# Kernel tuning notes

Hardware: AMD Instinct MI355X
Metric: run time of the kernel (lower is better)

The kernel has to match this reference:

```python
import jax, jax.numpy as jnp
import numpy as np
from jax import lax

H, MEM, AUX = 1024, 256, 16
S = MEM + AUX          # total_slots
B, T = 8, 4096
TOPK = 8               # top_k_binding
GAMMA, BETA, PTS = 0.92, 0.08, 0.4  # gamma, beta, prediction_torque_scale
RANK = 10              # coupling_rank == prediction_rank


def _inv_softplus(v):
    return float(np.log(np.expm1(max(float(v), 1e-6))))


def setup_inputs() -> dict:
    key = jax.random.key(0)
    ks = jax.random.split(key, 8)
    x = jax.random.normal(ks[0], (B, T, H), dtype=jnp.float32)
    # base basis: orthonormal columns in the first MEM slots (memory_dim < hidden_dim -> QR branch)
    q, _ = jnp.linalg.qr(jax.random.normal(ks[1], (H, MEM), dtype=jnp.float32))
    basis = jnp.zeros((H, S), jnp.float32).at[:, :MEM].set(q)
    return dict(
        x=x,
        basis=basis,
        tape_init_re=jax.random.normal(ks[2], (S,), dtype=jnp.float32) / S ** 0.5,
        tape_init_im=jax.random.normal(ks[3], (S,), dtype=jnp.float32) / S ** 0.5,
        eta_raw=jnp.asarray(_inv_softplus(0.08), jnp.float32),
        alpha=jnp.asarray(0.35, jnp.float32),
        torque_rotation=jnp.zeros((S,), jnp.float32),
        w_r=jnp.zeros((S,), jnp.float32),
        breadth_gate=jnp.zeros((S,), jnp.float32),
        epsilon_factor=jax.random.normal(ks[4], (S, RANK), dtype=jnp.float32) * 0.02,
        epsilon_scale=jnp.zeros((RANK,), jnp.float32),
        epsilon_diag=jnp.zeros((S,), jnp.float32),
        pred_factor=jax.random.normal(ks[5], (S, RANK), dtype=jnp.float32) * 0.02,
        pred_scale=jnp.zeros((RANK,), jnp.float32),
        pred_diag=jnp.zeros((S,), jnp.float32),
    )


def _forward(x, basis, tape_init_re, tape_init_im, eta_raw, alpha,
             torque_rotation, w_r, breadth_gate,
             epsilon_factor, epsilon_scale, epsilon_diag,
             pred_factor, pred_scale, pred_diag):
    active = jnp.arange(S) < MEM                      # base slots active (fixed population)
    amf = active.astype(jnp.float32)
    eta = jax.nn.softplus(eta_raw)
    # low-rank Hermitian coupling epsilon and prediction operator W_pred
    eps = (epsilon_factor * epsilon_scale) @ epsilon_factor.T + jnp.diag(epsilon_diag)
    wp = (pred_factor * pred_scale) @ pred_factor.T + jnp.diag(pred_diag)
    eps_c = eps.astype(jnp.complex64)
    wp_c = wp.astype(jnp.complex64)
    rot = jnp.exp(1j * torque_rotation.astype(jnp.complex64))  # torque phase rotation
    wr_gate = jax.nn.sigmoid(w_r)
    bg = jax.nn.sigmoid(breadth_gate)

    def renorm(tape):
        masked = tape * amf
        nrm = jnp.sqrt(jnp.maximum((jnp.abs(masked) ** 2).sum(-1, keepdims=True), 1e-16))
        return masked / nrm

    tape0 = (tape_init_re + 1j * tape_init_im) * amf   # aux slots zeroed as in _complex_tape_init
    tape0 = renorm(jnp.broadcast_to(tape0, (B, S)))

    def step(carry, x_t):
        tape, prev = carry                              # [B,S] complex64 each
        m = jnp.einsum('hs,bh->bs', basis, x_t)         # project into slot space
        mag = jnp.abs(m) * amf
        kth = lax.top_k(mag, TOPK)[0][:, -1:]           # top-k binding threshold
        inj = jnp.where((mag >= kth) & active, m, 0.0).astype(jnp.complex64)
        rotated = tape * rot
        drive = jnp.einsum('st,bt->bs', eps_c, rotated)  # coupling drive
        pred = jnp.einsum('st,bt->bs', wp_c, rotated)    # prediction torque
        new = (GAMMA * rotated + eta * drive + BETA * inj
               + PTS * 1j * pred + wr_gate * prev)
        new = renorm(new)
        y = x_t + alpha * jnp.einsum('hs,bs->bh', basis, bg * new.real)
        return (new, tape), y

    (_, _), ys = lax.scan(step, (tape0, tape0), jnp.swapaxes(x, 0, 1))
    return jnp.swapaxes(ys, 0, 1)


def reference(x, basis, tape_init_re, tape_init_im, eta_raw, alpha,
              torque_rotation, w_r, breadth_gate,
              epsilon_factor, epsilon_scale, epsilon_diag,
              pred_factor, pred_scale, pred_diag):
    return _forward(x, basis, tape_init_re, tape_init_im, eta_raw, alpha,
                    torque_rotation, w_r, breadth_gate,
                    epsilon_factor, epsilon_scale, epsilon_diag,
                    pred_factor, pred_scale, pred_diag)
```

## Files before the change

### kernel.cpp

```cpp
#include <hip/hip_runtime.h>
#include <cstdint>
#include <cstddef>

#define HD    1024
#define SLOTS 272
#define MEMS  256
#define BATCH 8
#define TT    4096
#define RR    (BATCH*TT)
#define RANKC 10

#define GAMMA 0.92f
#define BETA  0.08f
#define PTS   0.4f

typedef float f32x2 __attribute__((ext_vector_type(2)));
#define PKFMA(a, b, c) __builtin_elementwise_fma((a), (b), (c))

#define DPP_ADD(v, ctrl, rmask)                                                   \
    v += __int_as_float(__builtin_amdgcn_update_dpp(                              \
        0, __float_as_int(v), (ctrl), (rmask), 0xf, true))

__device__ __forceinline__ float wave_sum_bcast(float v)
{
    DPP_ADD(v, 0xB1,  0xf);
    DPP_ADD(v, 0x4E,  0xf);
    DPP_ADD(v, 0x141, 0xf);
    DPP_ADD(v, 0x140, 0xf);
    DPP_ADD(v, 0x142, 0xa);
    DPP_ADD(v, 0x143, 0xc);
    return __int_as_float(__builtin_amdgcn_readlane(__float_as_int(v), 63));
}

__global__ void prep_kernel(const float* __restrict__ t0re, const float* __restrict__ t0im,
                            const float* __restrict__ eta_raw,
                            const float* __restrict__ trot, const float* __restrict__ w_r,
                            const float* __restrict__ bgate,
                            const float* __restrict__ eps_scale, const float* __restrict__ pred_scale,
                            const float* __restrict__ eps_diag, const float* __restrict__ pred_diag,
                            float* __restrict__ consts, int* __restrict__ flags)
{
    __shared__ float red[MEMS];
    const int s = threadIdx.x;
    const float tr = t0re[s], ti = t0im[s];
    red[s] = tr * tr + ti * ti;
    __syncthreads();
    for (int off = 128; off > 0; off >>= 1) {
        if (s < off) red[s] += red[s + off];
        __syncthreads();
    }
    const float nrm = sqrtf(fmaxf(red[0], 1e-16f));
    const float eta = log1pf(expf(eta_raw[0]));
    const float rc = cosf(trot[s]), rs = sinf(trot[s]);
    const float c1 = GAMMA + eta * eps_diag[s];
    const float c2 = PTS * pred_diag[s];
    consts[0 * MEMS + s] = 1.0f / (1.0f + expf(-w_r[s]));
    consts[1 * MEMS + s] = 1.0f / (1.0f + expf(-bgate[s]));
    consts[2 * MEMS + s] = c1 * rc - c2 * rs;
    consts[3 * MEMS + s] = c1 * rs + c2 * rc;
    consts[4 * MEMS + s] = tr / nrm;
    consts[5 * MEMS + s] = ti / nrm;
    consts[6 * MEMS + s] = rc;
    consts[7 * MEMS + s] = rs;
    if (s == 0) {
        consts[8 * MEMS] = eta;
        int f1 = 0, f2 = 0;
        for (int k = 0; k < RANKC; ++k) {
            if (eps_scale[k]  != 0.0f) f1 = 1;
            if (pred_scale[k] != 0.0f) f2 = 1;
        }
        flags[0] = f1;
        flags[1] = f2;
    }
}

__global__ __launch_bounds__(256) void proj_kernel(const float* __restrict__ x,
                                                   const float* __restrict__ basis,
                                                   float* __restrict__ M)
{
    __shared__ float As[32][68];
    __shared__ float Bs[32][68];
    const int tid  = threadIdx.x;
    const int row0 = blockIdx.x * 64;
    const int col0 = blockIdx.y * 64;
    const int mt = tid >> 4, nt = tid & 15;
    float acc[4][4] = {};
    for (int k0 = 0; k0 < HD; k0 += 32) {
        {
            int q = tid, m = q >> 3, kq = q & 7;
            float4 a = *(const float4*)&x[(size_t)(row0 + m) * HD + k0 + kq * 4];
            As[kq * 4 + 0][m] = a.x; As[kq * 4 + 1][m] = a.y;
            As[kq * 4 + 2][m] = a.z; As[kq * 4 + 3][m] = a.w;
            q = tid + 256; m = q >> 3; kq = q & 7;
            float4 b = *(const float4*)&x[(size_t)(row0 + m) * HD + k0 + kq * 4];
            As[kq * 4 + 0][m] = b.x; As[kq * 4 + 1][m] = b.y;
            As[kq * 4 + 2][m] = b.z; As[kq * 4 + 3][m] = b.w;
            q = tid; int k = q >> 4; int nq = q & 15;
            float4 c = *(const float4*)&basis[(size_t)(k0 + k) * SLOTS + col0 + nq * 4];
            *(float4*)&Bs[k][nq * 4] = c;
            q = tid + 256; k = q >> 4; nq = q & 15;
            float4 d = *(const float4*)&basis[(size_t)(k0 + k) * SLOTS + col0 + nq * 4];
            *(float4*)&Bs[k][nq * 4] = d;
        }
        __syncthreads();
#pragma unroll
        for (int kk = 0; kk < 32; ++kk) {
            float4 a = *(const float4*)&As[kk][mt * 4];
            float4 b = *(const float4*)&Bs[kk][nt * 4];
            float av[4] = {a.x, a.y, a.z, a.w};
            float bv[4] = {b.x, b.y, b.z, b.w};
#pragma unroll
            for (int i = 0; i < 4; ++i)
#pragma unroll
                for (int j = 0; j < 4; ++j) acc[i][j] += av[i] * bv[j];
        }
        __syncthreads();
    }
#pragma unroll
    for (int i = 0; i < 4; ++i) {
        float4 o = {acc[i][0], acc[i][1], acc[i][2], acc[i][3]};
        *(float4*)&M[(size_t)(row0 + mt * 4 + i) * MEMS + col0 + nt * 4] = o;
    }
}

__global__ __launch_bounds__(64) void topk_kernel(float* __restrict__ M)
{
    const int r    = blockIdx.x;
    const int lane = threadIdx.x;
    float4 v = *(const float4*)&M[(size_t)r * MEMS + lane * 4];
    float vals[4] = {fabsf(v.x), fabsf(v.y), fabsf(v.z), fabsf(v.w)};
    float keep[4] = {vals[0], vals[1], vals[2], vals[3]};
    float kv = 0.0f;
#pragma unroll
    for (int it = 0; it < 8; ++it) {
        float lm = vals[0]; int li = 0;
#pragma unroll
        for (int j = 1; j < 4; ++j)
            if (vals[j] > lm) { lm = vals[j]; li = j; }
        float bm = lm; int bi = lane * 4 + li;
#pragma unroll
        for (int off = 1; off < 64; off <<= 1) {
            float om = __shfl_xor(bm, off);
            int   oi = __shfl_xor(bi, off);
            if (om > bm || (om == bm && oi < bi)) { bm = om; bi = oi; }
        }
        kv = bm;
        if ((bi >> 2) == lane) vals[bi & 3] = -1.0f;
    }
    float4 o;
    o.x = (keep[0] >= kv) ? BETA * v.x : 0.0f;
    o.y = (keep[1] >= kv) ? BETA * v.y : 0.0f;
    o.z = (keep[2] >= kv) ? BETA * v.z : 0.0f;
    o.w = (keep[3] >= kv) ? BETA * v.w : 0.0f;
    *(float4*)&M[(size_t)r * MEMS + lane * 4] = o;
}

__global__ __launch_bounds__(64) void scan_kernel(const float* __restrict__ M,
                                                  const float* __restrict__ consts,
                                                  const int* __restrict__ flags,
                                                  const float* __restrict__ eps_fac,
                                                  const float* __restrict__ eps_scale,
                                                  const float* __restrict__ eps_diag,
                                                  const float* __restrict__ pred_fac,
                                                  const float* __restrict__ pred_scale,
                                                  const float* __restrict__ pred_diag,
                                                  float* __restrict__ Wout)
{
    const int b    = blockIdx.x;
    const int lane = threadIdx.x;
    const int s0   = lane * 4;
    const int general = flags[0] | flags[1];
    const size_t base = (size_t)b * TT * MEMS + s0;

    if (!general) {
        f32x2 wrg[2], A2[2], B2[2], nB2[2];
        f32x2 wre[2], wim[2], qre[2], qim[2];
        {
            const float4 w4 = *(const float4*)&consts[0 * MEMS + s0];
            const float4 a4 = *(const float4*)&consts[2 * MEMS + s0];
            const float4 b4 = *(const float4*)&consts[3 * MEMS + s0];
            const float4 r4 = *(const float4*)&consts[4 * MEMS + s0];
            const float4 i4 = *(const float4*)&consts[5 * MEMS + s0];
            wrg[0] = {w4.x, w4.y};  wrg[1] = {w4.z, w4.w};
            A2[0]  = {a4.x, a4.y};  A2[1]  = {a4.z, a4.w};
            B2[0]  = {b4.x, b4.y};  B2[1]  = {b4.z, b4.w};
            nB2[0] = {-b4.x, -b4.y}; nB2[1] = {-b4.z, -b4.w};
            wre[0] = {r4.x, r4.y};  wre[1] = {r4.z, r4.w};
            wim[0] = {i4.x, i4.y};  wim[1] = {i4.z, i4.w};
            qre[0] = wre[0]; qre[1] = wre[1];
            qim[0] = wim[0]; qim[1] = wim[1];
        }
        float ssp;
        {
            const f32x2 p0 = PKFMA(wim[0], wim[0], wre[0] * wre[0]);
            const f32x2 p1 = PKFMA(wim[1], wim[1], wre[1] * wre[1]);
            const f32x2 pp = p0 + p1;
            ssp = pp.x + pp.y;
        }
        float4 mbuf[16];
#pragma unroll
        for (int j = 0; j < 16; ++j)
            mbuf[j] = *(const float4*)&M[base + (size_t)j * MEMS];
        for (int t0 = 0; t0 < TT; t0 += 16) {
#pragma unroll
            for (int j = 0; j < 16; ++j) {
                const int t = t0 + j;
                const float4 mc = mbuf[j];
                mbuf[j] = *(const float4*)&M[base + (size_t)(t + 16) * MEMS];
                const float stot = wave_sum_bcast(ssp);
                const float icv  = __builtin_amdgcn_rsqf(fmaxf(stot, 1e-16f));
                const f32x2 ic2  = {icv, icv};
                const f32x2 Lr0 = PKFMA(A2[0], wre[0], nB2[0] * wim[0]);
                const f32x2 Li0 = PKFMA(B2[0], wre[0], A2[0]  * wim[0]);
                const f32x2 Lr1 = PKFMA(A2[1], wre[1], nB2[1] * wim[1]);
                const f32x2 Li1 = PKFMA(B2[1], wre[1], A2[1]  * wim[1]);
                const f32x2 m0 = {mc.x, mc.y};
                const f32x2 m1 = {mc.z, mc.w};
                const f32x2 wqr0 = PKFMA(wrg[0], qre[0], m0);
                const f32x2 wqi0 = wrg[0] * qim[0];
                const f32x2 wqr1 = PKFMA(wrg[1], qre[1], m1);
                const f32x2 wqi1 = wrg[1] * qim[1];
                const f32x2 u1r0 = PKFMA(ic2, Lr0, wqr0);
                const f32x2 u1i0 = PKFMA(ic2, Li0, wqi0);
                const f32x2 u1r1 = PKFMA(ic2, Lr1, wqr1);
                const f32x2 u1i1 = PKFMA(ic2, Li1, wqi1);
                const f32x2 ps0 = PKFMA(u1i0, u1i0, u1r0 * u1r0);
                const f32x2 ps1 = PKFMA(u1i1, u1i1, u1r1 * u1r1);
                const f32x2 pp  = ps0 + ps1;
                const f32x2 nr0 = wre[0] * ic2, ni0 = wim[0] * ic2;
                const f32x2 nr1 = wre[1] * ic2, ni1 = wim[1] * ic2;
                const int tr = (t - 1) < 0 ? 0 : (t - 1);
                const float4 wq4 = {nr0.x, nr0.y, nr1.x, nr1.y};
                *(float4*)&Wout[base + (size_t)tr * MEMS] = wq4;
                qre[0] = nr0;  qim[0] = ni0;  qre[1] = nr1;  qim[1] = ni1;
                wre[0] = u1r0; wim[0] = u1i0; wre[1] = u1r1; wim[1] = u1i1;
                ssp = pp.x + pp.y;
            }
        }
        {
            const float stot = wave_sum_bcast(ssp);
            const float icv  = __builtin_amdgcn_rsqf(fmaxf(stot, 1e-16f));
            const float4 wq4 = {wre[0].x * icv, wre[0].y * icv,
                                wre[1].x * icv, wre[1].y * icv};
            *(float4*)&Wout[base + (size_t)(TT - 1) * MEMS] = wq4;
        }
        return;
    }

    float wr4[4], ur[4], ui[4], pr[4], pi[4];
    float rc4[4], rs4[4], ed4[4], pd4[4];
#pragma unroll
    for (int i = 0; i < 4; ++i) {
        wr4[i] = consts[0 * MEMS + s0 + i];
        ur[i]  = consts[4 * MEMS + s0 + i];
        ui[i]  = consts[5 * MEMS + s0 + i];
        pr[i] = ur[i]; pi[i] = ui[i];
        rc4[i] = consts[6 * MEMS + s0 + i];
        rs4[i] = consts[7 * MEMS + s0 + i];
        ed4[i] = eps_diag[s0 + i];
        pd4[i] = pred_diag[s0 + i];
    }
    const float eta  = consts[8 * MEMS];
    const int es_any = flags[0];
    const int ps_any = flags[1];
    float4 mbuf[4];
#pragma unroll
    for (int j = 0; j < 4; ++j)
        mbuf[j] = *(const float4*)&M[base + (size_t)j * MEMS];
    for (int t0 = 0; t0 < TT; t0 += 4) {
#pragma unroll
        for (int j = 0; j < 4; ++j) {
            const int t = t0 + j;
            const float4 mc = mbuf[j];
            mbuf[j] = *(const float4*)&M[base + (size_t)(t + 4) * MEMS];
            float rr[4], ri[4], nr[4], ni[4];
#pragma unroll
            for (int i = 0; i < 4; ++i) {
                rr[i] = ur[i] * rc4[i] - ui[i] * rs4[i];
                ri[i] = ur[i] * rs4[i] + ui[i] * rc4[i];
            }
            const float mv[4] = {mc.x, mc.y, mc.z, mc.w};
#pragma unroll
            for (int i = 0; i < 4; ++i) {
                nr[i] = GAMMA * rr[i] + wr4[i] * pr[i] + eta * ed4[i] * rr[i]
                        - PTS * pd4[i] * ri[i] + mv[i];
                ni[i] = GAMMA * ri[i] + wr4[i] * pi[i] + eta * ed4[i] * ri[i]
                        + PTS * pd4[i] * rr[i];
            }
            if (es_any) {
#pragma unroll
                for (int k = 0; k < RANKC; ++k) {
                    float u[4], prj = 0.0f, pij = 0.0f;
#pragma unroll
                    for (int i = 0; i < 4; ++i) {
                        u[i] = eps_fac[(size_t)(s0 + i) * RANKC + k];
                        prj = fmaf(u[i], rr[i], prj);
                        pij = fmaf(u[i], ri[i], pij);
                    }
                    prj = wave_sum_bcast(prj);
                    pij = wave_sum_bcast(pij);
                    const float sc = eta * eps_scale[k];
#pragma unroll
                    for (int i = 0; i < 4; ++i) {
                        nr[i] = fmaf(sc * u[i], prj, nr[i]);
                        ni[i] = fmaf(sc * u[i], pij, ni[i]);
                    }
                }
            }
            if (ps_any) {
#pragma unroll
                for (int k = 0; k < RANKC; ++k) {
                    float u[4], qrj = 0.0f, qij = 0.0f;
#pragma unroll
                    for (int i = 0; i < 4; ++i) {
                        u[i] = pred_fac[(size_t)(s0 + i) * RANKC + k];
                        qrj = fmaf(u[i], rr[i], qrj);
                        qij = fmaf(u[i], ri[i], qij);
                    }
                    qrj = wave_sum_bcast(qrj);
                    qij = wave_sum_bcast(qij);
                    const float sc = PTS * pred_scale[k];
#pragma unroll
                    for (int i = 0; i < 4; ++i) {
                        nr[i] = fmaf(-sc * u[i], qij, nr[i]);
                        ni[i] = fmaf( sc * u[i], qrj, ni[i]);
                    }
                }
            }
            float ss = 0.0f;
#pragma unroll
            for (int i = 0; i < 4; ++i) ss = fmaf(nr[i], nr[i], fmaf(ni[i], ni[i], ss));
            ss = wave_sum_bcast(ss);
            const float inv = __builtin_amdgcn_rsqf(fmaxf(ss, 1e-16f));
#pragma unroll
            for (int i = 0; i < 4; ++i) {
                pr[i] = ur[i]; pi[i] = ui[i];
                ur[i] = nr[i] * inv; ui[i] = ni[i] * inv;
            }
            const float4 wq = {ur[0], ur[1], ur[2], ur[3]};
            *(float4*)&Wout[base + (size_t)t * MEMS] = wq;
        }
    }
}

__global__ __launch_bounds__(256) void outp_kernel(const float* __restrict__ W,
                                                   const float* __restrict__ basis,
                                                   const float* __restrict__ x,
                                                   const float* __restrict__ alpha_p,
                                                   const float* __restrict__ consts,
                                                   float* __restrict__ y)
{
    __shared__ float As[32][68];
    __shared__ float Bs[32][68];
    const int tid  = threadIdx.x;
    const int row0 = blockIdx.x * 64;
    const int col0 = blockIdx.y * 64;
    const int mt = tid >> 4, nt = tid & 15;
    const float alpha = alpha_p[0];
    const float* bgc  = consts + MEMS;
    const int m0 = tid >> 3, m1 = (tid + 256) >> 3;
    const int kq0 = tid & 7;
    float acc[4][4] = {};
    for (int k0 = 0; k0 < MEMS; k0 += 32) {
        {
            const float4 bgv = *(const float4*)&bgc[k0 + kq0 * 4];
            const float bx = alpha * bgv.x, by = alpha * bgv.y;
            const float bz = alpha * bgv.z, bw = alpha * bgv.w;
            float4 a = *(const float4*)&W[(size_t)(row0 + m0) * MEMS + k0 + kq0 * 4];
            As[kq0 * 4 + 0][m0] = a.x; As[kq0 * 4 + 1][m0] = a.y;
            As[kq0 * 4 + 2][m0] = a.z; As[kq0 * 4 + 3][m0] = a.w;
            float4 b = *(const float4*)&W[(size_t)(row0 + m1) * MEMS + k0 + kq0 * 4];
            As[kq0 * 4 + 0][m1] = b.x; As[kq0 * 4 + 1][m1] = b.y;
            As[kq0 * 4 + 2][m1] = b.z; As[kq0 * 4 + 3][m1] = b.w;
            int q = tid; int n = q >> 3;
            float4 c = *(const float4*)&basis[(size_t)(col0 + n) * SLOTS + k0 + kq0 * 4];
            Bs[kq0 * 4 + 0][n] = c.x * bx; Bs[kq0 * 4 + 1][n] = c.y * by;
            Bs[kq0 * 4 + 2][n] = c.z * bz; Bs[kq0 * 4 + 3][n] = c.w * bw;
            q = tid + 256; n = q >> 3;
            float4 d = *(const float4*)&basis[(size_t)(col0 + n) * SLOTS + k0 + kq0 * 4];
            Bs[kq0 * 4 + 0][n] = d.x * bx; Bs[kq0 * 4 + 1][n] = d.y * by;
            Bs[kq0 * 4 + 2][n] = d.z * bz; Bs[kq0 * 4 + 3][n] = d.w * bw;
        }
        __syncthreads();
#pragma unroll
        for (int kk = 0; kk < 32; ++kk) {
            float4 a = *(const float4*)&As[kk][mt * 4];
            float4 b = *(const float4*)&Bs[kk][nt * 4];
            float av[4] = {a.x, a.y, a.z, a.w};
            float bv[4] = {b.x, b.y, b.z, b.w};
#pragma unroll
            for (int i = 0; i < 4; ++i)
#pragma unroll
                for (int j = 0; j < 4; ++j) acc[i][j] += av[i] * bv[j];
        }
        __syncthreads();
    }
#pragma unroll
    for (int i = 0; i < 4; ++i) {
        const size_t ro = (size_t)(row0 + mt * 4 + i) * HD + col0 + nt * 4;
        float4 xv = *(const float4*)&x[ro];
        float4 o  = {xv.x + acc[i][0], xv.y + acc[i][1],
                     xv.z + acc[i][2], xv.w + acc[i][3]};
        *(float4*)&y[ro] = o;
    }
}

extern "C" void kernel_launch(void* const* d_in, const int* in_sizes, int n_in,
                              void* d_out, int out_size, void* d_ws, size_t ws_size,
                              hipStream_t stream)
{
    const float* x          = (const float*)d_in[0];
    const float* basis      = (const float*)d_in[1];
    const float* t0re       = (const float*)d_in[2];
    const float* t0im       = (const float*)d_in[3];
    const float* eta_raw    = (const float*)d_in[4];
    const float* alpha      = (const float*)d_in[5];
    const float* trot       = (const float*)d_in[6];
    const float* w_r        = (const float*)d_in[7];
    const float* bgate      = (const float*)d_in[8];
    const float* eps_fac    = (const float*)d_in[9];
    const float* eps_scale  = (const float*)d_in[10];
    const float* eps_diag   = (const float*)d_in[11];
    const float* pred_fac   = (const float*)d_in[12];
    const float* pred_scale = (const float*)d_in[13];
    const float* pred_diag  = (const float*)d_in[14];
    float* out = (float*)d_out;

    const size_t szM = (size_t)RR * MEMS * sizeof(float);
    const size_t szW = szM;
    const size_t szC = 16384;

    char* ws = (char*)d_ws;
    float *Mbuf, *Wbuf, *cbuf;
    if (ws_size >= szM + szW + szC) {
        Mbuf = (float*)(ws);
        Wbuf = (float*)(ws + szM);
        cbuf = (float*)(ws + szM + szW);
    } else {
        Mbuf = (float*)d_out;
        Wbuf = (float*)(ws);
        cbuf = (float*)(ws + szW);
    }
    int* fbuf = (int*)(cbuf + 8 * MEMS + 16);

    prep_kernel<<<1, 256, 0, stream>>>(t0re, t0im, eta_raw, trot, w_r, bgate,
                                       eps_scale, pred_scale, eps_diag, pred_diag,
                                       cbuf, fbuf);
    proj_kernel<<<dim3(RR / 64, MEMS / 64), 256, 0, stream>>>(x, basis, Mbuf);
    topk_kernel<<<RR, 64, 0, stream>>>(Mbuf);
    scan_kernel<<<BATCH, 64, 0, stream>>>(Mbuf, cbuf, fbuf,
                                          eps_fac, eps_scale, eps_diag,
                                          pred_fac, pred_scale, pred_diag,
                                          Wbuf);
    outp_kernel<<<dim3(RR / 64, HD / 64), 256, 0, stream>>>(Wbuf, basis, x, alpha,
                                                            cbuf, out);
}
```

Before: 1.069 ms.

## Widen GEMM tiles to 64x256 and restructure scan normalization reduction

Both GEMM kernels (projection and output) switch from 64x64 tiles with K-step 32 to 64x256 tiles with K-step 16, and each thread now computes a 2x2 set of 4x4 sub-blocks. The aim is more data reuse per shared-memory load and fewer redundant reads of x and W. In the fast-path scan, the per-step norm computation is re-expressed algebraically: three partial dot products (L·L, L·W, W·W) are reduced together in one batched DPP pass, so the reduction is no longer on the serial dependency chain between steps. The cost is more registers in the GEMMs, which can lower occupancy, and slightly different floating-point rounding in the scan.

```diff
diff --git a/kernel.cpp b/kernel.cpp
--- a/kernel.cpp
+++ b/kernel.cpp
@@ -30,6 +30,18 @@
     DPP_ADD(v, 0x142, 0xa);
     DPP_ADD(v, 0x143, 0xc);
     return __int_as_float(__builtin_amdgcn_readlane(__float_as_int(v), 63));
+}
+
+__device__ __forceinline__ void wave_sum3(float& a, float& b, float& c)
+{
+#define L3(ctrl, rmask)                                                           \
+    DPP_ADD(a, ctrl, rmask); DPP_ADD(b, ctrl, rmask); DPP_ADD(c, ctrl, rmask);
+    L3(0xB1, 0xf) L3(0x4E, 0xf) L3(0x141, 0xf)
+    L3(0x140, 0xf) L3(0x142, 0xa) L3(0x143, 0xc)
+#undef L3
+    a = __int_as_float(__builtin_amdgcn_readlane(__float_as_int(a), 63));
+    b = __int_as_float(__builtin_amdgcn_readlane(__float_as_int(b), 63));
+    c = __int_as_float(__builtin_amdgcn_readlane(__float_as_int(c), 63));
 }
 
 __global__ void prep_kernel(const float* __restrict__ t0re, const float* __restrict__ t0im,
@@ -78,49 +90,61 @@
                                                    const float* __restrict__ basis,
                                                    float* __restrict__ M)
 {
-    __shared__ float As[32][68];
-    __shared__ float Bs[32][68];
+    __shared__ float As[16][64];
+    __shared__ float Bs[16][260];
     const int tid  = threadIdx.x;
     const int row0 = blockIdx.x * 64;
-    const int col0 = blockIdx.y * 64;
-    const int mt = tid >> 4, nt = tid & 15;
-    float acc[4][4] = {};
-    for (int k0 = 0; k0 < HD; k0 += 32) {
+    const int mt = tid >> 5;
+    const int nt = tid & 31;
+    const int ar = tid >> 2;
+    const int ak = (tid & 3) * 4;
+    const int bk = tid >> 4;
+    const int bn = (tid & 15) * 16;
+    float acc[2][2][4][4] = {};
+    for (int k0 = 0; k0 < HD; k0 += 16) {
         {
-            int q = tid, m = q >> 3, kq = q & 7;
-            float4 a = *(const float4*)&x[(size_t)(row0 + m) * HD + k0 + kq * 4];
-            As[kq * 4 + 0][m] = a.x; As[kq * 4 + 1][m] = a.y;
-            As[kq * 4 + 2][m] = a.z; As[kq * 4 + 3][m] = a.w;
-            q = tid + 256; m = q >> 3; kq = q & 7;
-            float4 b = *(const float4*)&x[(size_t)(row0 + m) * HD + k0 + kq * 4];
-            As[kq * 4 + 0][m] = b.x; As[kq * 4 + 1][m] = b.y;
-            As[kq * 4 + 2][m] = b.z; As[kq * 4 + 3][m] = b.w;
-            q = tid; int k = q >> 4; int nq = q & 15;
-            float4 c = *(const float4*)&basis[(size_t)(k0 + k) * SLOTS + col0 + nq * 4];
-            *(float4*)&Bs[k][nq * 4] = c;
-            q = tid + 256; k = q >> 4; nq = q & 15;
-            float4 d = *(const float4*)&basis[(size_t)(k0 + k) * SLOTS + col0 + nq * 4];
-            *(float4*)&Bs[k][nq * 4] = d;
+            const float4 av = *(const float4*)&x[(size_t)(row0 + ar) * HD + k0 + ak];
+            As[ak + 0][ar] = av.x; As[ak + 1][ar] = av.y;
+            As[ak + 2][ar] = av.z; As[ak + 3][ar] = av.w;
+#pragma unroll
+            for (int c = 0; c < 4; ++c) {
+                const float4 bv = *(const float4*)&basis[(size_t)(k0 + bk) * SLOTS + bn + c * 4];
+                *(float4*)&Bs[bk][bn + c * 4] = bv;
+            }
         }
         __syncthreads();
 #pragma unroll
-        for (int kk = 0; kk < 32; ++kk) {
-            float4 a = *(const float4*)&As[kk][mt * 4];
-            float4 b = *(const float4*)&Bs[kk][nt * 4];
-            float av[4] = {a.x, a.y, a.z, a.w};
-            float bv[4] = {b.x, b.y, b.z, b.w};
-#pragma unroll
-            for (int i = 0; i < 4; ++i)
-#pragma unroll
-                for (int j = 0; j < 4; ++j) acc[i][j] += av[i] * bv[j];
+        for (int kk = 0; kk < 16; ++kk) {
+            const float4 a0 = *(const float4*)&As[kk][mt * 4];
+            const float4 a1 = *(const float4*)&As[kk][32 + mt * 4];
+            const float4 b0 = *(const float4*)&Bs[kk][nt * 4];
+            const float4 b1 = *(const float4*)&Bs[kk][128 + nt * 4];
+            const float av[2][4] = {{a0.x, a0.y, a0.z, a0.w}, {a1.x, a1.y, a1.z, a1.w}};
+            const float bv[2][4] = {{b0.x, b0.y, b0.z, b0.w}, {b1.x, b1.y, b1.z, b1.w}};
+#pragma unroll
+            for (int p = 0; p < 2; ++p)
+#pragma unroll
+                for (int q = 0; q < 2; ++q)
+#pragma unroll
+                    for (int i = 0; i < 4; ++i)
+#pragma unroll
+                        for (int j = 0; j < 4; ++j)
+                            acc[p][q][i][j] += av[p][i] * bv[q][j];
         }
         __syncthreads();
     }
 #pragma unroll
-    for (int i = 0; i < 4; ++i) {
-        float4 o = {acc[i][0], acc[i][1], acc[i][2], acc[i][3]};
-        *(float4*)&M[(size_t)(row0 + mt * 4 + i) * MEMS + col0 + nt * 4] = o;
-    }
+    for (int p = 0; p < 2; ++p)
+#pragma unroll
+        for (int i = 0; i < 4; ++i) {
+            const int r = row0 + p * 32 + mt * 4 + i;
+#pragma unroll
+            for (int q = 0; q < 2; ++q) {
+                const float4 o = {acc[p][q][i][0], acc[p][q][i][1],
+                                  acc[p][q][i][2], acc[p][q][i][3]};
+                *(float4*)&M[(size_t)r * MEMS + q * 128 + nt * 4] = o;
+            }
+        }
 }
 
 __global__ __launch_bounds__(64) void topk_kernel(float* __restrict__ M)
@@ -173,7 +197,7 @@
     const size_t base = (size_t)b * TT * MEMS + s0;
 
     if (!general) {
-        f32x2 wrg[2], A2[2], B2[2], nB2[2];
+        f32x2 wrg[2], A2[2], B2[2];
         f32x2 wre[2], wim[2], qre[2], qim[2];
         {
             const float4 w4 = *(const float4*)&consts[0 * MEMS + s0];
@@ -184,19 +208,12 @@
             wrg[0] = {w4.x, w4.y};  wrg[1] = {w4.z, w4.w};
             A2[0]  = {a4.x, a4.y};  A2[1]  = {a4.z, a4.w};
             B2[0]  = {b4.x, b4.y};  B2[1]  = {b4.z, b4.w};
-            nB2[0] = {-b4.x, -b4.y}; nB2[1] = {-b4.z, -b4.w};
             wre[0] = {r4.x, r4.y};  wre[1] = {r4.z, r4.w};
             wim[0] = {i4.x, i4.y};  wim[1] = {i4.z, i4.w};
             qre[0] = wre[0]; qre[1] = wre[1];
             qim[0] = wim[0]; qim[1] = wim[1];
         }
-        float ssp;
-        {
-            const f32x2 p0 = PKFMA(wim[0], wim[0], wre[0] * wre[0]);
-            const f32x2 p1 = PKFMA(wim[1], wim[1], wre[1] * wre[1]);
-            const f32x2 pp = p0 + p1;
-            ssp = pp.x + pp.y;
-        }
+        float icv = 1.0f;
         float4 mbuf[16];
 #pragma unroll
         for (int j = 0; j < 16; ++j)
@@ -207,39 +224,41 @@
                 const int t = t0 + j;
                 const float4 mc = mbuf[j];
                 mbuf[j] = *(const float4*)&M[base + (size_t)(t + 16) * MEMS];
-                const float stot = wave_sum_bcast(ssp);
-                const float icv  = __builtin_amdgcn_rsqf(fmaxf(stot, 1e-16f));
-                const f32x2 ic2  = {icv, icv};
-                const f32x2 Lr0 = PKFMA(A2[0], wre[0], nB2[0] * wim[0]);
-                const f32x2 Li0 = PKFMA(B2[0], wre[0], A2[0]  * wim[0]);
-                const f32x2 Lr1 = PKFMA(A2[1], wre[1], nB2[1] * wim[1]);
-                const f32x2 Li1 = PKFMA(B2[1], wre[1], A2[1]  * wim[1]);
+                const f32x2 Lr0 = PKFMA(A2[0], wre[0], -(B2[0] * wim[0]));
+                const f32x2 Li0 = PKFMA(B2[0], wre[0],  A2[0] * wim[0]);
+                const f32x2 Lr1 = PKFMA(A2[1], wre[1], -(B2[1] * wim[1]));
+                const f32x2 Li1 = PKFMA(B2[1], wre[1],  A2[1] * wim[1]);
                 const f32x2 m0 = {mc.x, mc.y};
                 const f32x2 m1 = {mc.z, mc.w};
-                const f32x2 wqr0 = PKFMA(wrg[0], qre[0], m0);
-                const f32x2 wqi0 = wrg[0] * qim[0];
-                const f32x2 wqr1 = PKFMA(wrg[1], qre[1], m1);
-                const f32x2 wqi1 = wrg[1] * qim[1];
-                const f32x2 u1r0 = PKFMA(ic2, Lr0, wqr0);
-                const f32x2 u1i0 = PKFMA(ic2, Li0, wqi0);
-                const f32x2 u1r1 = PKFMA(ic2, Lr1, wqr1);
-                const f32x2 u1i1 = PKFMA(ic2, Li1, wqi1);
-                const f32x2 ps0 = PKFMA(u1i0, u1i0, u1r0 * u1r0);
-                const f32x2 ps1 = PKFMA(u1i1, u1i1, u1r1 * u1r1);
-                const f32x2 pp  = ps0 + ps1;
-                const f32x2 nr0 = wre[0] * ic2, ni0 = wim[0] * ic2;
-                const f32x2 nr1 = wre[1] * ic2, ni1 = wim[1] * ic2;
-                const int tr = (t - 1) < 0 ? 0 : (t - 1);
-                const float4 wq4 = {nr0.x, nr0.y, nr1.x, nr1.y};
-                *(float4*)&Wout[base + (size_t)tr * MEMS] = wq4;
-                qre[0] = nr0;  qim[0] = ni0;  qre[1] = nr1;  qim[1] = ni1;
-                wre[0] = u1r0; wim[0] = u1i0; wre[1] = u1r1; wim[1] = u1i1;
-                ssp = pp.x + pp.y;
+                const f32x2 Wr0 = PKFMA(wrg[0], qre[0], m0);
+                const f32x2 Wi0 = wrg[0] * qim[0];
+                const f32x2 Wr1 = PKFMA(wrg[1], qre[1], m1);
+                const f32x2 Wi1 = wrg[1] * qim[1];
+                f32x2 el = PKFMA(Li0, Li0, Lr0 * Lr0);
+                el = PKFMA(Lr1, Lr1, el); el = PKFMA(Li1, Li1, el);
+                float pl = el.x + el.y;
+                f32x2 ex = PKFMA(Li0, Wi0, Lr0 * Wr0);
+                ex = PKFMA(Lr1, Wr1, ex); ex = PKFMA(Li1, Wi1, ex);
+                float px2 = (ex.x + ex.y) * 2.0f;
+                f32x2 ew = PKFMA(Wi0, Wi0, Wr0 * Wr0);
+                ew = PKFMA(Wr1, Wr1, ew); ew = PKFMA(Wi1, Wi1, ew);
+                float pw = ew.x + ew.y;
+                wave_sum3(pl, px2, pw);
+                const f32x2 ic2 = {icv, icv};
+                const f32x2 sr0 = wre[0] * ic2, si0 = wim[0] * ic2;
+                const f32x2 sr1 = wre[1] * ic2, si1 = wim[1] * ic2;
+                const int trow = t ? (t - 1) : 0;
+                const float4 st4 = {sr0.x, sr0.y, sr1.x, sr1.y};
+                *(float4*)&Wout[base + (size_t)trow * MEMS] = st4;
+                const f32x2 w0r = PKFMA(ic2, Lr0, Wr0), w0i = PKFMA(ic2, Li0, Wi0);
+                const f32x2 w1r = PKFMA(ic2, Lr1, Wr1), w1i = PKFMA(ic2, Li1, Wi1);
+                const float nn = fmaf(fmaf(icv, pl, px2), icv, pw);
+                icv = __builtin_amdgcn_rsqf(fmaxf(nn, 1e-16f));
+                qre[0] = sr0; qim[0] = si0; qre[1] = sr1; qim[1] = si1;
+                wre[0] = w0r; wim[0] = w0i; wre[1] = w1r; wim[1] = w1i;
             }
         }
         {
-            const float stot = wave_sum_bcast(ssp);
-            const float icv  = __builtin_amdgcn_rsqf(fmaxf(stot, 1e-16f));
             const float4 wq4 = {wre[0].x * icv, wre[0].y * icv,
                                 wre[1].x * icv, wre[1].y * icv};
             *(float4*)&Wout[base + (size_t)(TT - 1) * MEMS] = wq4;
@@ -350,59 +369,68 @@
                                                    const float* __restrict__ consts,
                                                    float* __restrict__ y)
 {
-    __shared__ float As[32][68];
-    __shared__ float Bs[32][68];
+    __shared__ float As[16][64];
+    __shared__ float Bs[16][260];
     const int tid  = threadIdx.x;
     const int row0 = blockIdx.x * 64;
-    const int col0 = blockIdx.y * 64;
-    const int mt = tid >> 4, nt = tid & 15;
+    const int col0 = blockIdx.y * 256;
+    const int mt = tid >> 5;
+    const int nt = tid & 31;
+    const int ar = tid >> 2;
+    const int ak = (tid & 3) * 4;
     const float alpha = alpha_p[0];
     const float* bgc  = consts + MEMS;
-    const int m0 = tid >> 3, m1 = (tid + 256) >> 3;
-    const int kq0 = tid & 7;
-    float acc[4][4] = {};
-    for (int k0 = 0; k0 < MEMS; k0 += 32) {
+    float acc[2][2][4][4] = {};
+    for (int k0 = 0; k0 < MEMS; k0 += 16) {
         {
-            const float4 bgv = *(const float4*)&bgc[k0 + kq0 * 4];
-            const float bx = alpha * bgv.x, by = alpha * bgv.y;
-            const float bz = alpha * bgv.z, bw = alpha * bgv.w;
-            float4 a = *(const float4*)&W[(size_t)(row0 + m0) * MEMS + k0 + kq0 * 4];
-            As[kq0 * 4 + 0][m0] = a.x; As[kq0 * 4 + 1][m0] = a.y;
-            As[kq0 * 4 + 2][m0] = a.z; As[kq0 * 4 + 3][m0] = a.w;
-            float4 b = *(const float4*)&W[(size_t)(row0 + m1) * MEMS + k0 + kq0 * 4];
-            As[kq0 * 4 + 0][m1] = b.x; As[kq0 * 4 + 1][m1] = b.y;
-            As[kq0 * 4 + 2][m1] = b.z; As[kq0 * 4 + 3][m1] = b.w;
-            int q = tid; int n = q >> 3;
-            float4 c = *(const float4*)&basis[(size_t)(col0 + n) * SLOTS + k0 + kq0 * 4];
-            Bs[kq0 * 4 + 0][n] = c.x * bx; Bs[kq0 * 4 + 1][n] = c.y * by;
-            Bs[kq0 * 4 + 2][n] = c.z * bz; Bs[kq0 * 4 + 3][n] = c.w * bw;
-            q = tid + 256; n = q >> 3;
-            float4 d = *(const float4*)&basis[(size_t)(col0 + n) * SLOTS + k0 + kq0 * 4];
-            Bs[kq0 * 4 + 0][n] = d.x * bx; Bs[kq0 * 4 + 1][n] = d.y * by;
-            Bs[kq0 * 4 + 2][n] = d.z * bz; Bs[kq0 * 4 + 3][n] = d.w * bw;
+            const float4 av = *(const float4*)&W[(size_t)(row0 + ar) * MEMS + k0 + ak];
+            As[ak + 0][ar] = av.x; As[ak + 1][ar] = av.y;
+            As[ak + 2][ar] = av.z; As[ak + 3][ar] = av.w;
+#pragma unroll
+            for (int c = 0; c < 4; ++c) {
+                const float4 bv  = *(const float4*)&basis[(size_t)(col0 + tid) * SLOTS + k0 + c * 4];
+                const float4 bg4 = *(const float4*)&bgc[k0 + c * 4];
+                Bs[c * 4 + 0][tid] = bv.x * (alpha * bg4.x);
+                Bs[c * 4 + 1][tid] = bv.y * (alpha * bg4.y);
+                Bs[c * 4 + 2][tid] = bv.z * (alpha * bg4.z);
+                Bs[c * 4 + 3][tid] = bv.w * (alpha * bg4.w);
+            }
         }
         __syncthreads();
 #pragma unroll
-        for (int kk = 0; kk < 32; ++kk) {
-            float4 a = *(const float4*)&As[kk][mt * 4];
-            float4 b = *(const float4*)&Bs[kk][nt * 4];
-            float av[4] = {a.x, a.y, a.z, a.w};
-            float bv[4] = {b.x, b.y, b.z, b.w};
-#pragma unroll
-            for (int i = 0; i < 4; ++i)
-#pragma unroll
-                for (int j = 0; j < 4; ++j) acc[i][j] += av[i] * bv[j];
+        for (int kk = 0; kk < 16; ++kk) {
+            const float4 a0 = *(const float4*)&As[kk][mt * 4];
+            const float4 a1 = *(const float4*)&As[kk][32 + mt * 4];
+            const float4 b0 = *(const float4*)&Bs[kk][nt * 4];
+            const float4 b1 = *(const float4*)&Bs[kk][128 + nt * 4];
+            const float av[2][4] = {{a0.x, a0.y, a0.z, a0.w}, {a1.x, a1.y, a1.z, a1.w}};
+            const float bv[2][4] = {{b0.x, b0.y, b0.z, b0.w}, {b1.x, b1.y, b1.z, b1.w}};
+#pragma unroll
+            for (int p = 0; p < 2; ++p)
+#pragma unroll
+                for (int q = 0; q < 2; ++q)
+#pragma unroll
+                    for (int i = 0; i < 4; ++i)
+#pragma unroll
+                        for (int j = 0; j < 4; ++j)
+                            acc[p][q][i][j] += av[p][i] * bv[q][j];
         }
         __syncthreads();
     }
 #pragma unroll
-    for (int i = 0; i < 4; ++i) {
-        const size_t ro = (size_t)(row0 + mt * 4 + i) * HD + col0 + nt * 4;
-        float4 xv = *(const float4*)&x[ro];
-        float4 o  = {xv.x + acc[i][0], xv.y + acc[i][1],
-                     xv.z + acc[i][2], xv.w + acc[i][3]};
-        *(float4*)&y[ro] = o;
-    }
+    for (int p = 0; p < 2; ++p)
+#pragma unroll
+        for (int i = 0; i < 4; ++i) {
+            const int r = row0 + p * 32 + mt * 4 + i;
+#pragma unroll
+            for (int q = 0; q < 2; ++q) {
+                const size_t ro = (size_t)r * HD + col0 + q * 128 + nt * 4;
+                const float4 xv = *(const float4*)&x[ro];
+                const float4 o  = {xv.x + acc[p][q][i][0], xv.y + acc[p][q][i][1],
+                                   xv.z + acc[p][q][i][2], xv.w + acc[p][q][i][3]};
+                *(float4*)&y[ro] = o;
+            }
+        }
 }
 
 extern "C" void kernel_launch(void* const* d_in, const int* in_sizes, int n_in,
@@ -446,12 +474,12 @@
     prep_kernel<<<1, 256, 0, stream>>>(t0re, t0im, eta_raw, trot, w_r, bgate,
                                        eps_scale, pred_scale, eps_diag, pred_diag,
                                        cbuf, fbuf);
-    proj_kernel<<<dim3(RR / 64, MEMS / 64), 256, 0, stream>>>(x, basis, Mbuf);
+    proj_kernel<<<dim3(RR / 64, 1), 256, 0, stream>>>(x, basis, Mbuf);
     topk_kernel<<<RR, 64, 0, stream>>>(Mbuf);
     scan_kernel<<<BATCH, 64, 0, stream>>>(Mbuf, cbuf, fbuf,
                                           eps_fac, eps_scale, eps_diag,
                                           pred_fac, pred_scale, pred_diag,
                                           Wbuf);
-    outp_kernel<<<dim3(RR / 64, HD / 64), 256, 0, stream>>>(Wbuf, basis, x, alpha,
-                                                            cbuf, out);
-}
+    outp_kernel<<<dim3(RR / 64, HD / 256), 256, 0, stream>>>(Wbuf, basis, x, alpha,
+                                                             cbuf, out);
+}
```

Result: slower. 1.285 ms (+20.2%).
